# Optimization experiments

Measured on AMD Instinct MI355X. Metric: run time of the kernel, lower is better.

## Reference

```python
import jax, jax.numpy as jnp
import numpy as np

NUM_EMBEDDINGS = 1024
EMBEDDING_DIM = 64
COMMITMENT_COST = 0.25


def setup_inputs() -> dict:
    key = jax.random.key(0)
    k1, k2 = jax.random.split(key)
    inputs = jax.random.normal(k1, (32, 64, 64, EMBEDDING_DIM), dtype=jnp.float32)
    # nn.Embedding weight init: uniform(-1/K, 1/K)
    bound = 1.0 / NUM_EMBEDDINGS
    emb = jax.random.uniform(k2, (NUM_EMBEDDINGS, EMBEDDING_DIM), dtype=jnp.float32,
                             minval=-bound, maxval=bound)
    return {"inputs": inputs, "emb": emb}


def reference(inputs, emb):
    K, D = emb.shape
    flat = inputs.reshape(-1, D)                       # [N, D]
    # squared euclidean distances to all codes: [N, K]
    distances = (jnp.sum(flat ** 2, axis=1, keepdims=True)
                 + jnp.sum(emb ** 2, axis=1)
                 - 2.0 * flat @ emb.T)
    idx = jnp.argmin(distances, axis=1)                # [N]
    # direct gather instead of one-hot scatter + matmul (same math)
    quantized = emb[idx].reshape(inputs.shape)

    e_latent_loss = jnp.mean((jax.lax.stop_gradient(quantized) - inputs) ** 2)
    q_latent_loss = jnp.mean((quantized - jax.lax.stop_gradient(inputs)) ** 2)
    loss = q_latent_loss + COMMITMENT_COST * e_latent_loss

    # straight-through estimator
    quantized_st = inputs + jax.lax.stop_gradient(quantized - inputs)

    # avg one-hot probs == normalized code counts
    counts = jnp.zeros((K,), dtype=flat.dtype).at[idx].add(1.0)
    avg_probs = counts / flat.shape[0]
    perplexity = jnp.exp(-jnp.sum(avg_probs * jnp.log(avg_probs + 1e-10)))

    encoding_indices = idx.reshape(inputs.shape[:-1])
    return quantized_st, loss, perplexity, encoding_indices
```

## Files before the change

kernel.cpp:

```cpp
#include <hip/hip_runtime.h>


#define N_ROWS   131072
#define K_CODES  1024
#define DIM      64
#define OUT_LOSS 8388608
#define OUT_PERP 8388609
#define OUT_IDX  8388610

typedef __attribute__((ext_vector_type(16))) float fvec16;


__global__ __launch_bounds__(256) void embnorm_kernel(const float* __restrict__ emb,
                                                      float* __restrict__ norms) {
    int k = blockIdx.x * blockDim.x + threadIdx.x;
    if (k < K_CODES) {
        const float* e = emb + (size_t)k * DIM;
        float r[8];
#pragma unroll
        for (int j = 0; j < 8; ++j) r[j] = __fmul_rn(e[j], e[j]);
#pragma unroll
        for (int i = 8; i < DIM; i += 8)
#pragma unroll
            for (int j = 0; j < 8; ++j) r[j] = __fadd_rn(r[j], __fmul_rn(e[i + j], e[i + j]));
        norms[k] = __fadd_rn(__fadd_rn(__fadd_rn(r[0], r[1]), __fadd_rn(r[2], r[3])),
                             __fadd_rn(__fadd_rn(r[4], r[5]), __fadd_rn(r[6], r[7])));
    }
}

__global__ __launch_bounds__(256)
__attribute__((amdgpu_waves_per_eu(4, 4)))
void vq_kernel(const float* __restrict__ inp,
               const float* __restrict__ emb,
               const float* __restrict__ norms,
               float* __restrict__ out,
               unsigned int* __restrict__ counts,
               double* __restrict__ sse) {
    const int tid  = threadIdx.x;
    const int rloc = tid & 127;
    const int half = __builtin_amdgcn_readfirstlane(tid >> 7);
    const int row  = blockIdx.x * 128 + rloc;

    const float4* xp = reinterpret_cast<const float4*>(inp + (size_t)row * DIM);
#define DECLX(i) float4 x##i = xp[i];
    DECLX(0)  DECLX(1)  DECLX(2)  DECLX(3)
    DECLX(4)  DECLX(5)  DECLX(6)  DECLX(7)
    DECLX(8)  DECLX(9)  DECLX(10) DECLX(11)
    DECLX(12) DECLX(13) DECLX(14) DECLX(15)

    float r0 = __fmul_rn(x0.x, x0.x), r1 = __fmul_rn(x0.y, x0.y);
    float r2 = __fmul_rn(x0.z, x0.z), r3 = __fmul_rn(x0.w, x0.w);
    float r4 = __fmul_rn(x1.x, x1.x), r5 = __fmul_rn(x1.y, x1.y);
    float r6 = __fmul_rn(x1.z, x1.z), r7 = __fmul_rn(x1.w, x1.w);
#define S1ACC(e, o) \
    r0 = __fadd_rn(r0, __fmul_rn(x##e.x, x##e.x)); \
    r1 = __fadd_rn(r1, __fmul_rn(x##e.y, x##e.y)); \
    r2 = __fadd_rn(r2, __fmul_rn(x##e.z, x##e.z)); \
    r3 = __fadd_rn(r3, __fmul_rn(x##e.w, x##e.w)); \
    r4 = __fadd_rn(r4, __fmul_rn(x##o.x, x##o.x)); \
    r5 = __fadd_rn(r5, __fmul_rn(x##o.y, x##o.y)); \
    r6 = __fadd_rn(r6, __fmul_rn(x##o.z, x##o.z)); \
    r7 = __fadd_rn(r7, __fmul_rn(x##o.w, x##o.w));
    S1ACC(2, 3) S1ACC(4, 5) S1ACC(6, 7) S1ACC(8, 9)
    S1ACC(10, 11) S1ACC(12, 13) S1ACC(14, 15)
    const float s1 = __fadd_rn(__fadd_rn(__fadd_rn(r0, r1), __fadd_rn(r2, r3)),
                               __fadd_rn(__fadd_rn(r4, r5), __fadd_rn(r6, r7)));

    const int kbeg = half << 9;
    const float* ebase = emb + ((size_t)kbeg << 6);
    const float* np_   = norms + kbeg;
    float best = 3.402823466e38f;
    int   bidx = 0;

#pragma unroll 1
    for (int kk = 0; kk < 512; ++kk) {
        fvec16 e0, e1, e2, e3;
        asm volatile(
            "s_load_dwordx16 %0, %4, 0x0\n\t"
            "s_load_dwordx16 %1, %4, 0x40\n\t"
            "s_load_dwordx16 %2, %4, 0x80\n\t"
            "s_load_dwordx16 %3, %4, 0xc0\n\t"
            "s_waitcnt lgkmcnt(0)"
            : "=s"(e0), "=s"(e1), "=s"(e2), "=s"(e3)
            : "s"(ebase));
        float acc = 0.f;
#define FMA4(xi, ev, b) \
        acc = __builtin_fmaf(x##xi.x, ev[b + 0], acc); \
        acc = __builtin_fmaf(x##xi.y, ev[b + 1], acc); \
        acc = __builtin_fmaf(x##xi.z, ev[b + 2], acc); \
        acc = __builtin_fmaf(x##xi.w, ev[b + 3], acc);
        FMA4(0,  e0, 0) FMA4(1,  e0, 4) FMA4(2,  e0, 8)  FMA4(3,  e0, 12)
        FMA4(4,  e1, 0) FMA4(5,  e1, 4) FMA4(6,  e1, 8)  FMA4(7,  e1, 12)
        FMA4(8,  e2, 0) FMA4(9,  e2, 4) FMA4(10, e2, 8)  FMA4(11, e2, 12)
        FMA4(12, e3, 0) FMA4(13, e3, 4) FMA4(14, e3, 8)  FMA4(15, e3, 12)
        float Dk = __fsub_rn(__fadd_rn(s1, np_[kk]), __fmul_rn(2.0f, acc));
        if (Dk < best) { best = Dk; bidx = kbeg + kk; }
        ebase += DIM;
    }

    __shared__ float sbest[256];
    __shared__ int   sidx[256];
    __shared__ float red[256];
    sbest[tid] = best;
    sidx[tid]  = bidx;
    __syncthreads();

    float err = 0.f;
    if (tid < 128) {
        float ob = sbest[tid + 128];
        int   oi = sidx[tid + 128];
        if (ob < best) { best = ob; bidx = oi; }

        const float4* eb = reinterpret_cast<const float4*>(emb) + ((size_t)bidx << 4);
        float4* qo = reinterpret_cast<float4*>(out + (size_t)row * DIM);
#define EPI(i) { float4 ev = eb[i]; qo[i] = ev; \
    float dx = ev.x - x##i.x, dy = ev.y - x##i.y; \
    float dz = ev.z - x##i.z, dw = ev.w - x##i.w; \
    err += dx * dx + dy * dy + dz * dz + dw * dw; }
        EPI(0)  EPI(1)  EPI(2)  EPI(3)
        EPI(4)  EPI(5)  EPI(6)  EPI(7)
        EPI(8)  EPI(9)  EPI(10) EPI(11)
        EPI(12) EPI(13) EPI(14) EPI(15)

        out[OUT_IDX + row] = (float)bidx;
        atomicAdd(&counts[bidx], 1u);
    }

    red[tid] = err;
    __syncthreads();
#pragma unroll
    for (int s = 128; s > 0; s >>= 1) {
        if (tid < s) red[tid] += red[tid + s];
        __syncthreads();
    }
    if (tid == 0) atomicAdd(sse, (double)red[0]);
}

__global__ __launch_bounds__(1024) void finalize_kernel(const unsigned int* __restrict__ counts,
                                                        const double* __restrict__ sse,
                                                        float* __restrict__ out) {
    __shared__ double red[1024];
    const int t = threadIdx.x;
    double p = (double)counts[t] / (double)N_ROWS;
    red[t] = -p * log(p + 1e-10);
    __syncthreads();
#pragma unroll
    for (int s = 512; s > 0; s >>= 1) {
        if (t < s) red[t] += red[t + s];
        __syncthreads();
    }
    if (t == 0) {
        out[OUT_PERP] = (float)exp(red[0]);
        out[OUT_LOSS] = (float)(1.25 * (*sse) / (double)((size_t)N_ROWS * DIM));
    }
}

extern "C" void kernel_launch(void* const* d_in, const int* in_sizes, int n_in,
                              void* d_out, int out_size, void* d_ws, size_t ws_size,
                              hipStream_t stream) {
    const float* inp = (const float*)d_in[0];
    const float* emb = (const float*)d_in[1];
    float* out = (float*)d_out;

    double*       sse    = (double*)d_ws;
    unsigned int* counts = (unsigned int*)((char*)d_ws + 16);
    float*        norms  = (float*)((char*)d_ws + 4112);

    hipMemsetAsync(d_ws, 0, 4112, stream);
    embnorm_kernel<<<4, 256, 0, stream>>>(emb, norms);
    vq_kernel<<<1024, 256, 0, stream>>>(inp, emb, norms, out, counts, sse);
    finalize_kernel<<<1, 1024, 0, stream>>>(counts, sse, out);
}
```

Before: 386.7 us.

## Process two rows per thread to reuse scalar-loaded codebook vectors

Each thread now holds two input rows in registers and computes dot products for both against each codebook entry loaded via scalar loads, halving the number of s_load batches per computed distance. The grid is halved to 512 blocks and the occupancy hint drops from 4 to 2 waves per EU to fit the doubled register footprint. This trades latency hiding from fewer resident waves for better amortization of the scalar load and wait per code. The epilogue merges the two K-halves for both rows.

```diff
diff --git a/kernel.cpp b/kernel.cpp
--- a/kernel.cpp
+++ b/kernel.cpp
@@ -28,26 +28,10 @@
     }
 }
 
-__global__ __launch_bounds__(256)
-__attribute__((amdgpu_waves_per_eu(4, 4)))
-void vq_kernel(const float* __restrict__ inp,
-               const float* __restrict__ emb,
-               const float* __restrict__ norms,
-               float* __restrict__ out,
-               unsigned int* __restrict__ counts,
-               double* __restrict__ sse) {
-    const int tid  = threadIdx.x;
-    const int rloc = tid & 127;
-    const int half = __builtin_amdgcn_readfirstlane(tid >> 7);
-    const int row  = blockIdx.x * 128 + rloc;
-
-    const float4* xp = reinterpret_cast<const float4*>(inp + (size_t)row * DIM);
-#define DECLX(i) float4 x##i = xp[i];
-    DECLX(0)  DECLX(1)  DECLX(2)  DECLX(3)
-    DECLX(4)  DECLX(5)  DECLX(6)  DECLX(7)
-    DECLX(8)  DECLX(9)  DECLX(10) DECLX(11)
-    DECLX(12) DECLX(13) DECLX(14) DECLX(15)
-
+__device__ __forceinline__ float s1row(float4 x0, float4 x1, float4 x2, float4 x3,
+                                       float4 x4, float4 x5, float4 x6, float4 x7,
+                                       float4 x8, float4 x9, float4 x10, float4 x11,
+                                       float4 x12, float4 x13, float4 x14, float4 x15) {
     float r0 = __fmul_rn(x0.x, x0.x), r1 = __fmul_rn(x0.y, x0.y);
     float r2 = __fmul_rn(x0.z, x0.z), r3 = __fmul_rn(x0.w, x0.w);
     float r4 = __fmul_rn(x1.x, x1.x), r5 = __fmul_rn(x1.y, x1.y);
@@ -63,14 +47,50 @@
     r7 = __fadd_rn(r7, __fmul_rn(x##o.w, x##o.w));
     S1ACC(2, 3) S1ACC(4, 5) S1ACC(6, 7) S1ACC(8, 9)
     S1ACC(10, 11) S1ACC(12, 13) S1ACC(14, 15)
-    const float s1 = __fadd_rn(__fadd_rn(__fadd_rn(r0, r1), __fadd_rn(r2, r3)),
-                               __fadd_rn(__fadd_rn(r4, r5), __fadd_rn(r6, r7)));
-
-    const int kbeg = half << 9;
+#undef S1ACC
+    return __fadd_rn(__fadd_rn(__fadd_rn(r0, r1), __fadd_rn(r2, r3)),
+                     __fadd_rn(__fadd_rn(r4, r5), __fadd_rn(r6, r7)));
+}
+
+__global__ __launch_bounds__(256)
+__attribute__((amdgpu_waves_per_eu(2, 2)))
+void vq_kernel(const float* __restrict__ inp,
+               const float* __restrict__ emb,
+               const float* __restrict__ norms,
+               float* __restrict__ out,
+               unsigned int* __restrict__ counts,
+               double* __restrict__ sse) {
+    const int tid   = threadIdx.x;
+    const int lane  = tid & 63;
+    const int set   = __builtin_amdgcn_readfirstlane(tid >> 7);
+    const int khalf = __builtin_amdgcn_readfirstlane((tid >> 6) & 1);
+    const int row1  = blockIdx.x * 256 + set * 128 + lane;
+    const int row2  = row1 + 64;
+
+    const float4* ap = reinterpret_cast<const float4*>(inp + (size_t)row1 * DIM);
+    const float4* bp = reinterpret_cast<const float4*>(inp + (size_t)row2 * DIM);
+#define DECLX(i) float4 a##i = ap[i]; float4 b##i = bp[i];
+    DECLX(0)  DECLX(1)  DECLX(2)  DECLX(3)
+    DECLX(4)  DECLX(5)  DECLX(6)  DECLX(7)
+    DECLX(8)  DECLX(9)  DECLX(10) DECLX(11)
+    DECLX(12) DECLX(13) DECLX(14) DECLX(15)
+
+    const float s1a = s1row(a0, a1, a2, a3, a4, a5, a6, a7,
+                            a8, a9, a10, a11, a12, a13, a14, a15);
+    const float s1b = s1row(b0, b1, b2, b3, b4, b5, b6, b7,
+                            b8, b9, b10, b11, b12, b13, b14, b15);
+
+    const int kbeg = khalf << 9;
     const float* ebase = emb + ((size_t)kbeg << 6);
     const float* np_   = norms + kbeg;
-    float best = 3.402823466e38f;
-    int   bidx = 0;
+    float bestA = 3.402823466e38f, bestB = 3.402823466e38f;
+    int   bidxA = 0, bidxB = 0;
+
+#define FM4(acc, xv, ev, b) \
+    acc = __builtin_fmaf(xv.x, ev[b + 0], acc); \
+    acc = __builtin_fmaf(xv.y, ev[b + 1], acc); \
+    acc = __builtin_fmaf(xv.z, ev[b + 2], acc); \
+    acc = __builtin_fmaf(xv.w, ev[b + 3], acc);
 
 #pragma unroll 1
     for (int kk = 0; kk < 512; ++kk) {
@@ -83,47 +103,67 @@
             "s_waitcnt lgkmcnt(0)"
             : "=s"(e0), "=s"(e1), "=s"(e2), "=s"(e3)
             : "s"(ebase));
-        float acc = 0.f;
-#define FMA4(xi, ev, b) \
-        acc = __builtin_fmaf(x##xi.x, ev[b + 0], acc); \
-        acc = __builtin_fmaf(x##xi.y, ev[b + 1], acc); \
-        acc = __builtin_fmaf(x##xi.z, ev[b + 2], acc); \
-        acc = __builtin_fmaf(x##xi.w, ev[b + 3], acc);
-        FMA4(0,  e0, 0) FMA4(1,  e0, 4) FMA4(2,  e0, 8)  FMA4(3,  e0, 12)
-        FMA4(4,  e1, 0) FMA4(5,  e1, 4) FMA4(6,  e1, 8)  FMA4(7,  e1, 12)
-        FMA4(8,  e2, 0) FMA4(9,  e2, 4) FMA4(10, e2, 8)  FMA4(11, e2, 12)
-        FMA4(12, e3, 0) FMA4(13, e3, 4) FMA4(14, e3, 8)  FMA4(15, e3, 12)
-        float Dk = __fsub_rn(__fadd_rn(s1, np_[kk]), __fmul_rn(2.0f, acc));
-        if (Dk < best) { best = Dk; bidx = kbeg + kk; }
+        float accA = 0.f, accB = 0.f;
+        FM4(accA, a0,  e0, 0)  FM4(accB, b0,  e0, 0)
+        FM4(accA, a1,  e0, 4)  FM4(accB, b1,  e0, 4)
+        FM4(accA, a2,  e0, 8)  FM4(accB, b2,  e0, 8)
+        FM4(accA, a3,  e0, 12) FM4(accB, b3,  e0, 12)
+        FM4(accA, a4,  e1, 0)  FM4(accB, b4,  e1, 0)
+        FM4(accA, a5,  e1, 4)  FM4(accB, b5,  e1, 4)
+        FM4(accA, a6,  e1, 8)  FM4(accB, b6,  e1, 8)
+        FM4(accA, a7,  e1, 12) FM4(accB, b7,  e1, 12)
+        FM4(accA, a8,  e2, 0)  FM4(accB, b8,  e2, 0)
+        FM4(accA, a9,  e2, 4)  FM4(accB, b9,  e2, 4)
+        FM4(accA, a10, e2, 8)  FM4(accB, b10, e2, 8)
+        FM4(accA, a11, e2, 12) FM4(accB, b11, e2, 12)
+        FM4(accA, a12, e3, 0)  FM4(accB, b12, e3, 0)
+        FM4(accA, a13, e3, 4)  FM4(accB, b13, e3, 4)
+        FM4(accA, a14, e3, 8)  FM4(accB, b14, e3, 8)
+        FM4(accA, a15, e3, 12) FM4(accB, b15, e3, 12)
+        float nk = np_[kk];
+        float DkA = __fsub_rn(__fadd_rn(s1a, nk), __fmul_rn(2.0f, accA));
+        float DkB = __fsub_rn(__fadd_rn(s1b, nk), __fmul_rn(2.0f, accB));
+        if (DkA < bestA) { bestA = DkA; bidxA = kbeg + kk; }
+        if (DkB < bestB) { bestB = DkB; bidxB = kbeg + kk; }
         ebase += DIM;
     }
 
-    __shared__ float sbest[256];
-    __shared__ int   sidx[256];
+    __shared__ float sb1[256], sb2[256];
+    __shared__ int   si1[256], si2[256];
     __shared__ float red[256];
-    sbest[tid] = best;
-    sidx[tid]  = bidx;
+    sb1[tid] = bestA; si1[tid] = bidxA;
+    sb2[tid] = bestB; si2[tid] = bidxB;
     __syncthreads();
 
     float err = 0.f;
-    if (tid < 128) {
-        float ob = sbest[tid + 128];
-        int   oi = sidx[tid + 128];
-        if (ob < best) { best = ob; bidx = oi; }
-
-        const float4* eb = reinterpret_cast<const float4*>(emb) + ((size_t)bidx << 4);
-        float4* qo = reinterpret_cast<float4*>(out + (size_t)row * DIM);
-#define EPI(i) { float4 ev = eb[i]; qo[i] = ev; \
-    float dx = ev.x - x##i.x, dy = ev.y - x##i.y; \
-    float dz = ev.z - x##i.z, dw = ev.w - x##i.w; \
-    err += dx * dx + dy * dy + dz * dz + dw * dw; }
+    if ((tid & 64) == 0) {
+        { float ob = sb1[tid + 64]; int oi = si1[tid + 64];
+          if (ob < bestA) { bestA = ob; bidxA = oi; } }
+        { float ob = sb2[tid + 64]; int oi = si2[tid + 64];
+          if (ob < bestB) { bestB = ob; bidxB = oi; } }
+
+        const float4* eA = reinterpret_cast<const float4*>(emb) + ((size_t)bidxA << 4);
+        const float4* eB = reinterpret_cast<const float4*>(emb) + ((size_t)bidxB << 4);
+        float4* qA = reinterpret_cast<float4*>(out + (size_t)row1 * DIM);
+        float4* qB = reinterpret_cast<float4*>(out + (size_t)row2 * DIM);
+#define EPI(i) \
+        { float4 ev = eA[i]; qA[i] = ev; \
+          float dx = ev.x - a##i.x, dy = ev.y - a##i.y; \
+          float dz = ev.z - a##i.z, dw = ev.w - a##i.w; \
+          err += dx * dx + dy * dy + dz * dz + dw * dw; } \
+        { float4 ev = eB[i]; qB[i] = ev; \
+          float dx = ev.x - b##i.x, dy = ev.y - b##i.y; \
+          float dz = ev.z - b##i.z, dw = ev.w - b##i.w; \
+          err += dx * dx + dy * dy + dz * dz + dw * dw; }
         EPI(0)  EPI(1)  EPI(2)  EPI(3)
         EPI(4)  EPI(5)  EPI(6)  EPI(7)
         EPI(8)  EPI(9)  EPI(10) EPI(11)
         EPI(12) EPI(13) EPI(14) EPI(15)
 
-        out[OUT_IDX + row] = (float)bidx;
-        atomicAdd(&counts[bidx], 1u);
+        out[OUT_IDX + row1] = (float)bidxA;
+        out[OUT_IDX + row2] = (float)bidxB;
+        atomicAdd(&counts[bidxA], 1u);
+        atomicAdd(&counts[bidxB], 1u);
     }
 
     red[tid] = err;
@@ -168,6 +208,6 @@
 
     hipMemsetAsync(d_ws, 0, 4112, stream);
     embnorm_kernel<<<4, 256, 0, stream>>>(emb, norms);
-    vq_kernel<<<1024, 256, 0, stream>>>(inp, emb, norms, out, counts, sse);
+    vq_kernel<<<512, 256, 0, stream>>>(inp, emb, norms, out, counts, sse);
     finalize_kernel<<<1, 1024, 0, stream>>>(counts, sse, out);
 }
```

New measurement: 376.1 us. 1.03x faster.
